# Optimization experiments

Measured on AMD Instinct MI355X. Metric: run time of the kernel, lower is better.

## Reference

```python
import jax, jax.numpy as jnp
import numpy as np

VOCAB, EMB, HID, FF, NCLS = 1000, 32, 32, 16, 7
T, B = 512, 512


def setup_inputs() -> dict:
    key = jax.random.key(0)
    ks = jax.random.split(key, 10)
    s = 1.0 / np.sqrt(HID)
    return {
        "x": jax.random.randint(ks[0], (T, B), 0, VOCAB, dtype=jnp.int64)
        if jax.config.jax_enable_x64 else jax.random.randint(ks[0], (T, B), 0, VOCAB, dtype=jnp.int32),
        "emb": jax.random.normal(ks[1], (VOCAB, EMB), dtype=jnp.float32),
        "W_ih": jax.random.uniform(ks[2], (4 * HID, EMB), minval=-s, maxval=s, dtype=jnp.float32),
        "W_hh": jax.random.uniform(ks[3], (4 * HID, HID), minval=-s, maxval=s, dtype=jnp.float32),
        "b_ih": jax.random.uniform(ks[4], (4 * HID,), minval=-s, maxval=s, dtype=jnp.float32),
        "b_hh": jax.random.uniform(ks[5], (4 * HID,), minval=-s, maxval=s, dtype=jnp.float32),
        "W1": jax.random.uniform(ks[6], (FF, HID), minval=-s, maxval=s, dtype=jnp.float32),
        "b1": jax.random.uniform(ks[7], (FF,), minval=-s, maxval=s, dtype=jnp.float32),
        "W2": jax.random.uniform(ks[8], (NCLS, FF), minval=-s, maxval=s, dtype=jnp.float32),
        "b2": jax.random.uniform(ks[9], (NCLS,), minval=-s, maxval=s, dtype=jnp.float32),
    }


def _lstm(xg, W_hh):
    # xg: (T, B, 4H) precomputed input-to-gate projections (incl. both biases)
    Bn = xg.shape[1]
    h0 = jnp.zeros((Bn, HID), xg.dtype)
    c0 = jnp.zeros((Bn, HID), xg.dtype)

    def step(carry, xg_t):
        h, c = carry
        g = xg_t + h @ W_hh.T  # (B, 4H)
        i, f, gg, o = jnp.split(g, 4, axis=-1)  # PyTorch gate order i,f,g,o
        i = jax.nn.sigmoid(i)
        f = jax.nn.sigmoid(f)
        gg = jnp.tanh(gg)
        o = jax.nn.sigmoid(o)
        c = f * c + i * gg
        h = o * jnp.tanh(c)
        return (h, c), h

    _, hs = jax.lax.scan(step, (h0, c0), xg)
    return hs  # (T, B, H)


def reference(x, emb, W_ih, W_hh, b_ih, b_hh, W1, b1, W2, b2):
    e = emb[x]  # (T, B, EMB) embedding lookup
    xg = jnp.einsum('tbe,ge->tbg', e, W_ih) + b_ih + b_hh  # (T, B, 4H)
    hs = _lstm(xg, W_hh)  # (T, B, H)
    z = jax.nn.relu(jnp.einsum('tbh,fh->tbf', hs, W1) + b1)  # (T, B, FF)
    logits = jnp.einsum('tbf,cf->tbc', z, W2) + b2  # (T, B, NCLS)
    # torch F.softmax with dim=None on a 3D tensor softmaxes over dim 0
    return jax.nn.softmax(logits, axis=0)
```

## Files before the change

kernel.cpp:

```cpp
#include <hip/hip_runtime.h>
#include <math.h>

#define TT    512
#define BB    512
#define HID   32
#define EMB   32
#define FFD   16
#define NCLS  7
#define VOCABN 1000

__device__ __forceinline__ float rl(float v, int k) {
    return __int_as_float(__builtin_amdgcn_readlane(__float_as_int(v), k));
}
__device__ __forceinline__ float fast_rcp(float x) {
#if defined(__has_builtin)
#if __has_builtin(__builtin_amdgcn_rcpf)
    return __builtin_amdgcn_rcpf(x);
#else
    return 1.0f / x;
#endif
#else
    return 1.0f / x;
#endif
}
__device__ __forceinline__ float sigf(float x) { return fast_rcp(1.0f + __expf(-x)); }
__device__ __forceinline__ float tanh_fast(float x) { return 2.0f * sigf(2.0f * x) - 1.0f; }

__global__ __launch_bounds__(64) void build_xg(
    const float* __restrict__ emb, const float* __restrict__ W_ih,
    const float* __restrict__ b_ih, const float* __restrict__ b_hh,
    float2* __restrict__ tab)
{
    const int v = blockIdx.x;
    const int j = threadIdx.x;
    const float* e  = emb + v * EMB;
    const float* w0 = W_ih + j * EMB;
    const float* w1 = W_ih + (j + 64) * EMB;
    float a0 = b_ih[j]      + b_hh[j];
    float a1 = b_ih[j + 64] + b_hh[j + 64];
    #pragma unroll
    for (int k = 0; k < EMB; ++k) {
        const float ek = e[k];
        a0 = fmaf(w0[k], ek, a0);
        a1 = fmaf(w1[k], ek, a1);
    }
    tab[v * 64 + j] = make_float2(a0, a1);
}

__global__ __launch_bounds__(64, 1) void lstm_rec(
    const int* __restrict__ x, const float2* __restrict__ tab,
    const float* __restrict__ W_hh, float* __restrict__ hsout)
{
    const int b  = blockIdx.x;
    const int j  = threadIdx.x;
    const int m  = j & 31;
    const bool lo = j < 32;

    __shared__ float sh[8 * HID];

    float whhA[HID], whhB[HID];
    #pragma unroll
    for (int k = 0; k < HID; k += 4) {
        float4 a;
        a = *(const float4*)(W_hh + j * HID + k);        whhA[k]=a.x; whhA[k+1]=a.y; whhA[k+2]=a.z; whhA[k+3]=a.w;
        a = *(const float4*)(W_hh + (j + 64) * HID + k); whhB[k]=a.x; whhB[k+1]=a.y; whhB[k+2]=a.z; whhB[k+3]=a.w;
    }
    #define PIN16(A, base) \
        asm volatile("" : "+v"((A)[(base)+0]), "+v"((A)[(base)+1]), "+v"((A)[(base)+2]), "+v"((A)[(base)+3]), \
                          "+v"((A)[(base)+4]), "+v"((A)[(base)+5]), "+v"((A)[(base)+6]), "+v"((A)[(base)+7]), \
                          "+v"((A)[(base)+8]), "+v"((A)[(base)+9]), "+v"((A)[(base)+10]), "+v"((A)[(base)+11]), \
                          "+v"((A)[(base)+12]), "+v"((A)[(base)+13]), "+v"((A)[(base)+14]), "+v"((A)[(base)+15]))
    PIN16(whhA, 0); PIN16(whhA, 16);
    PIN16(whhB, 0); PIN16(whhB, 16);
    #undef PIN16

    float h = 0.f, c = 0.f;
    float* hrow0 = hsout + (size_t)b * TT * HID;

    int xc = x[2 * BB + b], xd = x[3 * BB + b];
    float2 xg  = tab[(size_t)x[b] * 64 + j];
    float2 xg1 = tab[(size_t)x[1 * BB + b] * 64 + j];

    for (int t8 = 0; t8 < TT / 8; ++t8) {
        #pragma unroll
        for (int u = 0; u < 8; ++u) {
            const int t = t8 * 8 + u;
            float2 xg2 = tab[(size_t)xc * 64 + j];
            const int tn = (t + 4 < TT) ? (t + 4) : (TT - 1);
            const int xnew = x[tn * BB + b];

            float hs[HID];
            #pragma unroll
            for (int k = 0; k < HID; ++k) hs[k] = rl(h, k);

            float p0 = xg.x, p1 = 0.f, q0 = xg.y, q1 = 0.f;
            #pragma unroll
            for (int k = 0; k < HID; k += 2) {
                p0 = fmaf(whhA[k],   hs[k],   p0); p1 = fmaf(whhA[k+1], hs[k+1], p1);
                q0 = fmaf(whhB[k],   hs[k],   q0); q1 = fmaf(whhB[k+1], hs[k+1], q1);
            }
            const float accA = p0 + p1, accB = q0 + q1;

            const float actA = sigf(accA);
            const float sB   = lo ? 2.0f * accB : accB;
            const float sgB  = sigf(sB);
            const float actB = lo ? 2.0f * sgB - 1.0f : sgB;
            const float oA = __shfl_xor(actA, 32);
            const float oB = __shfl_xor(actB, 32);
            const float gi = lo ? actA : oA;
            const float gf = lo ? oA   : actA;
            const float gg = lo ? actB : oB;
            const float go = lo ? oB   : actB;
            c = fmaf(gf, c, gi * gg);
            h = go * tanh_fast(c);

            if (lo) sh[u * HID + m] = h;
            xg = xg1; xg1 = xg2; xc = xd; xd = xnew;
        }
        const float4 v = *(const float4*)(sh + j * 4);
        *(float4*)(hrow0 + t8 * 8 * HID + j * 4) = v;
    }
}

__global__ __launch_bounds__(256) void ff_softmax(
    const float* __restrict__ hs,
    const float* __restrict__ W1, const float* __restrict__ b1,
    const float* __restrict__ W2, const float* __restrict__ b2,
    float* __restrict__ out)
{
    const int b    = blockIdx.x;
    const int tid  = threadIdx.x;
    const int lane = tid & 63, wv = tid >> 6;
    const int t0   = tid * 2;

    __shared__ float redM[4][NCLS];
    __shared__ float redS[4][NCLS];

    float4 hv[16];
    const float4* hb = (const float4*)(hs + ((size_t)b * TT + t0) * HID);
    #pragma unroll
    for (int q = 0; q < 16; ++q) hv[q] = hb[q];

    float lg[2][NCLS];
    #pragma unroll
    for (int r = 0; r < 2; ++r) {
        const float* hr = (const float*)(hv + 8 * r);
        float z[FFD];
        #pragma unroll
        for (int f = 0; f < FFD; ++f) {
            float a = b1[f];
            #pragma unroll
            for (int k = 0; k < HID; ++k) a = fmaf(W1[f * HID + k], hr[k], a);
            z[f] = fmaxf(a, 0.f);
        }
        #pragma unroll
        for (int cc = 0; cc < NCLS; ++cc) {
            float a = b2[cc];
            #pragma unroll
            for (int f = 0; f < FFD; ++f) a = fmaf(W2[cc * FFD + f], z[f], a);
            lg[r][cc] = a;
        }
    }

    float M[NCLS], S[NCLS];
    #pragma unroll
    for (int cc = 0; cc < NCLS; ++cc) {
        float mm = fmaxf(lg[0][cc], lg[1][cc]);
        #pragma unroll
        for (int off = 32; off; off >>= 1) mm = fmaxf(mm, __shfl_xor(mm, off));
        if (lane == 0) redM[wv][cc] = mm;
    }
    __syncthreads();
    #pragma unroll
    for (int cc = 0; cc < NCLS; ++cc)
        M[cc] = fmaxf(fmaxf(redM[0][cc], redM[1][cc]), fmaxf(redM[2][cc], redM[3][cc]));

    #pragma unroll
    for (int cc = 0; cc < NCLS; ++cc) {
        float ss = __expf(lg[0][cc] - M[cc]) + __expf(lg[1][cc] - M[cc]);
        #pragma unroll
        for (int off = 32; off; off >>= 1) ss += __shfl_xor(ss, off);
        if (lane == 0) redS[wv][cc] = ss;
    }
    __syncthreads();
    #pragma unroll
    for (int cc = 0; cc < NCLS; ++cc)
        S[cc] = (redS[0][cc] + redS[1][cc]) + (redS[2][cc] + redS[3][cc]);

    #pragma unroll
    for (int r = 0; r < 2; ++r) {
        float* o = out + ((size_t)(t0 + r) * BB + b) * NCLS;
        #pragma unroll
        for (int cc = 0; cc < NCLS; ++cc)
            o[cc] = __expf(lg[r][cc] - M[cc]) * fast_rcp(S[cc]);
    }
}

template <bool TAB>
__global__ __launch_bounds__(64) void lstm_all(
    const int* __restrict__ x, const float* __restrict__ emb,
    const float* __restrict__ W_ih, const float* __restrict__ W_hh,
    const float* __restrict__ b_ih, const float* __restrict__ b_hh,
    const float* __restrict__ W1, const float* __restrict__ b1,
    const float* __restrict__ W2, const float* __restrict__ b2,
    const float2* __restrict__ tab, float* __restrict__ out)
{
    const int b  = blockIdx.x;
    const int j  = threadIdx.x;
    const int m  = j & 31;
    const bool lo = j < 32;
    const int rA = j, rB = j + 64;

    float whhA[HID], whhB[HID];
    #pragma unroll
    for (int k = 0; k < HID; k += 4) {
        float4 a;
        a = *(const float4*)(W_hh + rA * HID + k); whhA[k]=a.x; whhA[k+1]=a.y; whhA[k+2]=a.z; whhA[k+3]=a.w;
        a = *(const float4*)(W_hh + rB * HID + k); whhB[k]=a.x; whhB[k+1]=a.y; whhB[k+2]=a.z; whhB[k+3]=a.w;
    }
    float wihA[HID], wihB[HID];
    float biasA = 0.f, biasB = 0.f;
    if constexpr (!TAB) {
        #pragma unroll
        for (int k = 0; k < HID; k += 4) {
            float4 a;
            a = *(const float4*)(W_ih + rA * HID + k); wihA[k]=a.x; wihA[k+1]=a.y; wihA[k+2]=a.z; wihA[k+3]=a.w;
            a = *(const float4*)(W_ih + rB * HID + k); wihB[k]=a.x; wihB[k+1]=a.y; wihB[k+2]=a.z; wihB[k+3]=a.w;
        }
        biasA = b_ih[rA] + b_hh[rA];
        biasB = b_ih[rB] + b_hh[rB];
    }
    const int f16 = j & 15;
    float w1r[HID];
    #pragma unroll
    for (int k = 0; k < HID; ++k) w1r[k] = W1[f16 * HID + k];
    const int cls = j & 7;
    const int c7  = (cls < NCLS) ? cls : 0;
    float w2r[FFD];
    #pragma unroll
    for (int f = 0; f < FFD; ++f) w2r[f] = W2[c7 * FFD + f];
    const float b1v = b1[f16];
    const float b2v = b2[c7];

    float h = 0.f, c = 0.f;
    float mrun = -3.0e38f, srun = 0.f;

    auto gates = [&](float accA, float accB) {
        const float actA = sigf(accA);
        const float sB   = lo ? 2.0f * accB : accB;
        const float sgB  = sigf(sB);
        const float actB = lo ? 2.0f * sgB - 1.0f : sgB;
        const float oA = __shfl_xor(actA, 32);
        const float oB = __shfl_xor(actB, 32);
        const float gi = lo ? actA : oA;
        const float gf = lo ? oA   : actA;
        const float gg = lo ? actB : oB;
        const float go = lo ? oB   : actB;
        c = fmaf(gf, c, gi * gg);
        h = go * tanh_fast(c);
    };

    auto ff_head = [&](int t_out, const float* hsv) {
        float z0 = b1v, z1 = 0.f;
        #pragma unroll
        for (int k = 0; k < HID; k += 2) {
            z0 = fmaf(w1r[k],     hsv[k],     z0);
            z1 = fmaf(w1r[k + 1], hsv[k + 1], z1);
        }
        const float z = fmaxf(z0 + z1, 0.0f);
        float lgv = b2v;
        #pragma unroll
        for (int f = 0; f < FFD; ++f) lgv = fmaf(w2r[f], rl(z, f), lgv);
        const float mn = fmaxf(mrun, lgv);
        srun = fmaf(srun, __expf(mrun - mn), __expf(lgv - mn));
        mrun = mn;
        if (j < NCLS) out[(t_out * BB + b) * NCLS + j] = lgv;
    };

    int xvn1 = x[1 * BB + b];
    int xvn2 = x[2 * BB + b];
    float2 xg = make_float2(0.f, 0.f);
    float eA = 0.f;
    if constexpr (TAB) xg = tab[(size_t)x[b] * 64 + j];
    else               eA = emb[x[b] * EMB + m];

    if constexpr (TAB) {
        gates(xg.x, xg.y);
    } else {
        float es[EMB];
        #pragma unroll
        for (int k = 0; k < EMB; ++k) es[k] = rl(eA, k);
        float p0 = biasA, p1 = 0.f, q0 = biasB, q1 = 0.f;
        #pragma unroll
        for (int k = 0; k < EMB; k += 2) {
            p0 = fmaf(wihA[k],   es[k],   p0); p1 = fmaf(wihA[k+1], es[k+1], p1);
            q0 = fmaf(wihB[k],   es[k],   q0); q1 = fmaf(wihB[k+1], es[k+1], q1);
        }
        gates(p0 + p1, q0 + q1);
    }
    if constexpr (TAB) xg = tab[(size_t)xvn1 * 64 + j];
    else               eA = emb[xvn1 * EMB + m];
    xvn1 = xvn2;
    xvn2 = x[3 * BB + b];

    for (int t = 1; t < TT; ++t) {
        float2 xg_n = make_float2(0.f, 0.f);
        float  e_n  = 0.f;
        if (t + 1 < TT) {
            if constexpr (TAB) xg_n = tab[(size_t)xvn1 * 64 + j];
            else               e_n  = emb[xvn1 * EMB + m];
        }
        const int xv_n3 = (t + 3 < TT) ? x[(t + 3) * BB + b] : 0;

        float hsv[HID];
        #pragma unroll
        for (int k = 0; k < HID; ++k) hsv[k] = rl(h, k);

        ff_head(t - 1, hsv);

        float p0, p1 = 0.f, q0, q1 = 0.f;
        if constexpr (TAB) { p0 = xg.x; q0 = xg.y; }
        else               { p0 = biasA; q0 = biasB; }
        if constexpr (!TAB) {
            float es[EMB];
            #pragma unroll
            for (int k = 0; k < EMB; ++k) es[k] = rl(eA, k);
            #pragma unroll
            for (int k = 0; k < EMB; k += 2) {
                p0 = fmaf(wihA[k],   es[k],   p0); p1 = fmaf(wihA[k+1], es[k+1], p1);
                q0 = fmaf(wihB[k],   es[k],   q0); q1 = fmaf(wihB[k+1], es[k+1], q1);
            }
        }
        #pragma unroll
        for (int k = 0; k < HID; k += 2) {
            p0 = fmaf(whhA[k],   hsv[k],   p0); p1 = fmaf(whhA[k+1], hsv[k+1], p1);
            q0 = fmaf(whhB[k],   hsv[k],   q0); q1 = fmaf(whhB[k+1], hsv[k+1], q1);
        }
        gates(p0 + p1, q0 + q1);

        xg = xg_n; eA = e_n; xvn1 = xvn2; xvn2 = xv_n3;
    }

    {
        float hsv[HID];
        #pragma unroll
        for (int k = 0; k < HID; ++k) hsv[k] = rl(h, k);
        ff_head(TT - 1, hsv);
    }

    #pragma unroll 1
    for (int cc = 0; cc < NCLS; ++cc) {
        const float mc = rl(mrun, cc);
        const float sc = rl(srun, cc);
        const float ic = 1.0f / sc;
        #pragma unroll
        for (int i = 0; i < TT / 64; ++i) {
            const int t = j + 64 * i;
            const int a = (t * BB + b) * NCLS + cc;
            out[a] = __expf(out[a] - mc) * ic;
        }
    }
}

extern "C" void kernel_launch(void* const* d_in, const int* in_sizes, int n_in,
                              void* d_out, int out_size, void* d_ws, size_t ws_size,
                              hipStream_t stream) {
    const int*   x   = (const int*)  d_in[0];
    const float* emb = (const float*)d_in[1];
    const float* Wih = (const float*)d_in[2];
    const float* Whh = (const float*)d_in[3];
    const float* bih = (const float*)d_in[4];
    const float* bhh = (const float*)d_in[5];
    const float* W1  = (const float*)d_in[6];
    const float* b1  = (const float*)d_in[7];
    const float* W2  = (const float*)d_in[8];
    const float* b2  = (const float*)d_in[9];
    float* out = (float*)d_out;

    const size_t tab_bytes = (size_t)VOCABN * 128 * sizeof(float);
    const size_t hs_off    = 524288;
    const size_t hs_bytes  = (size_t)BB * TT * HID * sizeof(float);
    if (ws_size >= hs_off + hs_bytes) {
        float2* tab = (float2*)d_ws;
        float*  hs  = (float*)((char*)d_ws + hs_off);
        build_xg<<<VOCABN, 64, 0, stream>>>(emb, Wih, bih, bhh, tab);
        lstm_rec<<<BB, 64, 0, stream>>>(x, tab, Whh, hs);
        ff_softmax<<<BB, 256, 0, stream>>>(hs, W1, b1, W2, b2, out);
    } else if (ws_size >= tab_bytes) {
        float2* tab = (float2*)d_ws;
        build_xg<<<VOCABN, 64, 0, stream>>>(emb, Wih, bih, bhh, tab);
        lstm_all<true><<<BB, 64, 0, stream>>>(x, emb, Wih, Whh, bih, bhh,
                                              W1, b1, W2, b2, tab, out);
    } else {
        lstm_all<false><<<BB, 64, 0, stream>>>(x, emb, Wih, Whh, bih, bhh,
                                               W1, b1, W2, b2, nullptr, out);
    }
}
```

Measured before the change: 289.4 us.

## Batch-prefetch LSTM gate inputs per 8-step block and use permlane32 swap

Replaces the rolling 2-step prefetch of embedding-projection rows with a block scheme: one block of eight table rows is held while the next block's rows and the token ids two blocks ahead are loaded. The cross-half exchange of gate activations switches from __shfl_xor to the permlane32_swap builtin when available, aiming to avoid the LDS-backed permute latency inside the serial recurrence. The recurrent dot product also uses four accumulators instead of two to shorten the FMA dependency chain. The costs are higher register pressure from the 16 prefetched float2 values, and reliance on the swap builtin's return semantics for correctness.

```diff
diff --git a/kernel.cpp b/kernel.cpp
--- a/kernel.cpp
+++ b/kernel.cpp
@@ -25,6 +25,20 @@
 }
 __device__ __forceinline__ float sigf(float x) { return fast_rcp(1.0f + __expf(-x)); }
 __device__ __forceinline__ float tanh_fast(float x) { return 2.0f * sigf(2.0f * x) - 1.0f; }
+
+__device__ __forceinline__ float xhalf_swap(float v) {
+#if defined(__has_builtin)
+#if __has_builtin(__builtin_amdgcn_permlane32_swap)
+    const unsigned u = __float_as_uint(v);
+    auto r = __builtin_amdgcn_permlane32_swap(u, u, false, false);
+    return __uint_as_float((r[0] ^ r[1]) ^ u);
+#else
+    return __shfl_xor(v, 32);
+#endif
+#else
+    return __shfl_xor(v, 32);
+#endif
+}
 
 __global__ __launch_bounds__(64) void build_xg(
     const float* __restrict__ emb, const float* __restrict__ W_ih,
@@ -77,36 +91,55 @@
     float h = 0.f, c = 0.f;
     float* hrow0 = hsout + (size_t)b * TT * HID;
 
-    int xc = x[2 * BB + b], xd = x[3 * BB + b];
-    float2 xg  = tab[(size_t)x[b] * 64 + j];
-    float2 xg1 = tab[(size_t)x[1 * BB + b] * 64 + j];
+    int xiB[8];
+    float2 cxg[8];
+    {
+        int xi0[8];
+        #pragma unroll
+        for (int u = 0; u < 8; ++u) xi0[u] = x[u * BB + b];
+        #pragma unroll
+        for (int u = 0; u < 8; ++u) xiB[u] = x[(8 + u) * BB + b];
+        #pragma unroll
+        for (int u = 0; u < 8; ++u) cxg[u] = tab[(size_t)xi0[u] * 64 + j];
+    }
 
     for (int t8 = 0; t8 < TT / 8; ++t8) {
+        float2 nxg[8];
+        #pragma unroll
+        for (int u = 0; u < 8; ++u) nxg[u] = tab[(size_t)xiB[u] * 64 + j];
+        int xiN[8];
+        const int nb2 = (t8 + 2 < TT / 8) ? (t8 + 2) * 8 : 0;
+        #pragma unroll
+        for (int u = 0; u < 8; ++u) xiN[u] = x[(nb2 + u) * BB + b];
+
         #pragma unroll
         for (int u = 0; u < 8; ++u) {
-            const int t = t8 * 8 + u;
-            float2 xg2 = tab[(size_t)xc * 64 + j];
-            const int tn = (t + 4 < TT) ? (t + 4) : (TT - 1);
-            const int xnew = x[tn * BB + b];
-
             float hs[HID];
             #pragma unroll
             for (int k = 0; k < HID; ++k) hs[k] = rl(h, k);
 
-            float p0 = xg.x, p1 = 0.f, q0 = xg.y, q1 = 0.f;
-            #pragma unroll
-            for (int k = 0; k < HID; k += 2) {
-                p0 = fmaf(whhA[k],   hs[k],   p0); p1 = fmaf(whhA[k+1], hs[k+1], p1);
-                q0 = fmaf(whhB[k],   hs[k],   q0); q1 = fmaf(whhB[k+1], hs[k+1], q1);
+            float p0 = cxg[u].x, p1 = 0.f, p2 = 0.f, p3 = 0.f;
+            float q0 = cxg[u].y, q1 = 0.f, q2 = 0.f, q3 = 0.f;
+            #pragma unroll
+            for (int k = 0; k < HID; k += 4) {
+                p0 = fmaf(whhA[k],   hs[k],   p0);
+                p1 = fmaf(whhA[k+1], hs[k+1], p1);
+                p2 = fmaf(whhA[k+2], hs[k+2], p2);
+                p3 = fmaf(whhA[k+3], hs[k+3], p3);
+                q0 = fmaf(whhB[k],   hs[k],   q0);
+                q1 = fmaf(whhB[k+1], hs[k+1], q1);
+                q2 = fmaf(whhB[k+2], hs[k+2], q2);
+                q3 = fmaf(whhB[k+3], hs[k+3], q3);
             }
-            const float accA = p0 + p1, accB = q0 + q1;
+            const float accA = (p0 + p1) + (p2 + p3);
+            const float accB = (q0 + q1) + (q2 + q3);
 
             const float actA = sigf(accA);
             const float sB   = lo ? 2.0f * accB : accB;
             const float sgB  = sigf(sB);
             const float actB = lo ? 2.0f * sgB - 1.0f : sgB;
-            const float oA = __shfl_xor(actA, 32);
-            const float oB = __shfl_xor(actB, 32);
+            const float oA = xhalf_swap(actA);
+            const float oB = xhalf_swap(actB);
             const float gi = lo ? actA : oA;
             const float gf = lo ? oA   : actA;
             const float gg = lo ? actB : oB;
@@ -115,10 +148,12 @@
             h = go * tanh_fast(c);
 
             if (lo) sh[u * HID + m] = h;
-            xg = xg1; xg1 = xg2; xc = xd; xd = xnew;
         }
         const float4 v = *(const float4*)(sh + j * 4);
         *(float4*)(hrow0 + t8 * 8 * HID + j * 4) = v;
+
+        #pragma unroll
+        for (int u = 0; u < 8; ++u) { cxg[u] = nxg[u]; xiB[u] = xiN[u]; }
     }
 }
 
```

After: 257.8 us. 10.9% less time.
